# Kernel optimization log

Measured on AMD Instinct MI355X. Metric: run time of the kernel, lower is better.

Reference implementation:

```python
import jax, jax.numpy as jnp
import numpy as np

OMEGA_0 = 30.0  # SIREN frequency from config.kernel.omega_0


def setup_inputs() -> dict:
    key = jax.random.key(0)
    ks = jax.random.split(key, 8)
    B, Ci, Co, L, H = 8, 64, 64, 8192, 32
    x = jax.random.normal(ks[0], (B, Ci, L), dtype=jnp.float32)
    # SIREN-style kernel-net params (Linear(1,H) -> sin -> Linear(H,H) -> sin -> Linear(H, Co*Ci))
    w1 = jax.random.uniform(ks[1], (1, H), jnp.float32, -1.0, 1.0)
    b1 = jax.random.uniform(ks[2], (H,), jnp.float32, -1.0, 1.0)
    c = np.sqrt(6.0 / H) / OMEGA_0
    w2 = jax.random.uniform(ks[3], (H, H), jnp.float32, -c, c)
    b2 = jax.random.uniform(ks[4], (H,), jnp.float32, -c, c)
    w3 = jax.random.uniform(ks[5], (H, Co * Ci), jnp.float32, -c, c)
    b3 = jax.random.uniform(ks[6], (Co * Ci,), jnp.float32, -c, c)
    bias = jnp.zeros((Co,), dtype=jnp.float32)  # CKConv bias init: fill_(0.0)
    return {"x": x, "w1": w1, "b1": b1, "w2": w2, "b2": b2,
            "w3": w3, "b3": b3, "bias": bias}


def reference(x, w1, b1, w2, b2, w3, b3, bias):
    B, Ci, L = x.shape
    Co = bias.shape[0]
    # 1. relative positions in [-1, 1], one per input sample
    rel = jnp.linspace(-1.0, 1.0, L).astype(x.dtype)[:, None]        # (L, 1)
    # 2. SIREN kernel net -> continuous kernel sampled at L positions
    h = jnp.sin(OMEGA_0 * (rel @ w1 + b1))                            # (L, H)
    h = jnp.sin(OMEGA_0 * (h @ w2 + b2))                              # (L, H)
    k = (h @ w3 + b3)                                                 # (L, Co*Ci)
    kernel = k.T.reshape(Co, Ci, L)                                   # (Co, Ci, L)
    # 3. causal full-length conv1d. torch's causal_padding (left zero-pad of
    #    x by K-1, plus a left zero on an even-length kernel) + conv1d
    #    (cross-correlation) is mathematically y[t] = sum_{tau<=t} x[t-tau] *
    #    kernel_flipped[tau], i.e. a causal linear convolution with the
    #    time-reversed kernel. Computed exactly via zero-padded FFT (N=2L >=
    #    L+L-1, so no circular wraparound) instead of O(L^2) direct conv.
    kr = kernel[:, :, ::-1]                                           # flip time axis
    N = 2 * L
    Xf = jnp.fft.rfft(x, n=N, axis=-1)                                # (B, Ci, N/2+1)
    Kf = jnp.fft.rfft(kr, n=N, axis=-1)                               # (Co, Ci, N/2+1)
    Yf = jnp.einsum('bif,oif->bof', Xf, Kf)                           # contract in-channels
    y = jnp.fft.irfft(Yf, n=N, axis=-1)[:, :, :L]                     # (B, Co, L)
    return y + bias[None, :, None]
```

## Files before the change

kernel.cpp:

```cpp
#include <hip/hip_runtime.h>


#define LSEQ   8192
#define N2     8192
#define HDIM   32
#define NB     33
#define NROWS  512
#define NFREQ  8193
#define FSTRIDE 8208
#define FBLK   8
#define FTH    1024
#define OMEGA0 30.0f
#define TWOPI  6.283185307179586f

#define IDX(i) ((i) + ((i) >> 4))
#define BR(k)  ((int)(__brev((unsigned)(k)) >> 19))

__device__ __forceinline__ void build_table(float2* Tq, int tid)
{
    for (int t = tid; t <= 1024; t += FTH) {
        float s, c;
        __sincosf(TWOPI * (float)t / 8192.0f, &s, &c);
        Tq[t] = make_float2(c, s);
    }
}

__device__ __forceinline__ void fft8192_core8(float* re, float* im,
                                              const float2* Tq, int tid)
{
    const float RC = 0.70710678118654752f;
    #pragma unroll
    for (int p = 10; p >= 1; p -= 3) {
        int m = 1 << p;
        int tmul = 1 << (10 - p);
        __syncthreads();
        for (int u = tid; u < 1024; u += FTH) {
            int j = u & (m - 1);
            int base = ((u >> p) << (p + 3)) + j;
            float xr[8], xi[8];
            #pragma unroll
            for (int q = 0; q < 8; ++q) {
                int ix = IDX(base + q * m);
                xr[q] = re[ix]; xi[q] = im[ix];
            }
            float t0r=xr[0]+xr[4], t0i=xi[0]+xi[4];
            float t1r=xr[0]-xr[4], t1i=xi[0]-xi[4];
            float t2r=xr[2]+xr[6], t2i=xi[2]+xi[6];
            float t3r=xr[2]-xr[6], t3i=xi[2]-xi[6];
            float E0r=t0r+t2r, E0i=t0i+t2i;
            float E2r=t0r-t2r, E2i=t0i-t2i;
            float E1r=t1r+t3i, E1i=t1i-t3r;
            float E3r=t1r-t3i, E3i=t1i+t3r;
            float s0r=xr[1]+xr[5], s0i=xi[1]+xi[5];
            float s1r=xr[1]-xr[5], s1i=xi[1]-xi[5];
            float s2r=xr[3]+xr[7], s2i=xi[3]+xi[7];
            float s3r=xr[3]-xr[7], s3i=xi[3]-xi[7];
            float O0r=s0r+s2r, O0i=s0i+s2i;
            float O2r=s0r-s2r, O2i=s0i-s2i;
            float O1r=s1r+s3i, O1i=s1i-s3r;
            float O3r=s1r-s3i, O3i=s1i+s3r;
            float u1r=(O1r+O1i)*RC, u1i=(O1i-O1r)*RC;
            float u2r=O2i,          u2i=-O2r;
            float u3r=(O3i-O3r)*RC, u3i=-(O3r+O3i)*RC;
            float X0r=E0r+O0r, X0i=E0i+O0i;
            float X4r=E0r-O0r, X4i=E0i-O0i;
            float X1r=E1r+u1r, X1i=E1i+u1i;
            float X5r=E1r-u1r, X5i=E1i-u1i;
            float X2r=E2r+u2r, X2i=E2i+u2i;
            float X6r=E2r-u2r, X6i=E2i-u2i;
            float X3r=E3r+u3r, X3i=E3i+u3i;
            float X7r=E3r-u3r, X7i=E3i-u3i;
            float2 tq = Tq[j * tmul];
            float w1r = tq.x,               w1i = -tq.y;
            float w2r = w1r*w1r - w1i*w1i,  w2i = 2.f*w1r*w1i;
            float w3r = w2r*w1r - w2i*w1i,  w3i = w2r*w1i + w2i*w1r;
            float w4r = w2r*w2r - w2i*w2i,  w4i = 2.f*w2r*w2i;
            float w5r = w4r*w1r - w4i*w1i,  w5i = w4r*w1i + w4i*w1r;
            float w6r = w3r*w3r - w3i*w3i,  w6i = 2.f*w3r*w3i;
            float w7r = w4r*w3r - w4i*w3i,  w7i = w4r*w3i + w4i*w3r;
            int i0=IDX(base),       i1=IDX(base+m),   i2=IDX(base+2*m), i3=IDX(base+3*m);
            int i4=IDX(base+4*m),   i5=IDX(base+5*m), i6=IDX(base+6*m), i7=IDX(base+7*m);
            re[i0]=X0r;                     im[i0]=X0i;
            re[i1]=X4r*w4r - X4i*w4i;       im[i1]=X4r*w4i + X4i*w4r;
            re[i2]=X2r*w2r - X2i*w2i;       im[i2]=X2r*w2i + X2i*w2r;
            re[i3]=X6r*w6r - X6i*w6i;       im[i3]=X6r*w6i + X6i*w6r;
            re[i4]=X1r*w1r - X1i*w1i;       im[i4]=X1r*w1i + X1i*w1r;
            re[i5]=X5r*w5r - X5i*w5i;       im[i5]=X5r*w5i + X5i*w5r;
            re[i6]=X3r*w3r - X3i*w3i;       im[i6]=X3r*w3i + X3i*w3r;
            re[i7]=X7r*w7r - X7i*w7i;       im[i7]=X7r*w7i + X7i*w7r;
        }
    }
    __syncthreads();
    for (int u = tid; u < 4096; u += FTH) {
        int a = IDX(2 * u), b = IDX(2 * u + 1);
        float ar = re[a], ai = im[a];
        float br = re[b], bi = im[b];
        re[a] = ar + br; im[a] = ai + bi;
        re[b] = ar - br; im[b] = ai - bi;
    }
    __syncthreads();
}

__global__ __launch_bounds__(FTH) void fwd_kernel(
    const float* __restrict__ x,
    const float* __restrict__ w1, const float* __restrict__ b1,
    const float* __restrict__ w2, const float* __restrict__ b2,
    const float* __restrict__ w3, const float* __restrict__ b3,
    float* __restrict__ Hf, float* __restrict__ XYf, float* __restrict__ M2)
{
    int blk = blockIdx.x;
    int tid = threadIdx.x;

    if (blk >= NB + NROWS) {
        int idx = (blk - (NB + NROWS)) * FTH + tid;
        if (idx < NB * 64 * 64) {
            int o = idx & 63;
            int i = (idx >> 6) & 63;
            int r = idx >> 12;
            M2[idx] = (r < HDIM) ? w3[r * 4096 + o * 64 + i] : b3[o * 64 + i];
        }
        return;
    }

    __shared__ float re[8704], im[8704];
    __shared__ float2 Tq[1025];
    build_table(Tq, tid);

    float* outF;
    long long orow;
    if (blk < NB) {
        int r = blk;
        for (int n = tid; n < 4096; n += FTH) {
            re[IDX(n + 4096)] = 0.0f;  im[IDX(n + 4096)] = 0.0f;
        }
        if (r < HDIM) {
            for (int t = tid; t < LSEQ; t += FTH) {
                float rel = -1.0f + 2.0f * (float)t / (float)(LSEQ - 1);
                float acc = b2[r];
                #pragma unroll 8
                for (int j = 0; j < HDIM; ++j)
                    acc = fmaf(sinf(OMEGA0 * fmaf(rel, w1[j], b1[j])), w2[j * HDIM + r], acc);
                float g = sinf(OMEGA0 * acc);
                int s = LSEQ - 1 - t;
                if (s & 1) im[IDX(s >> 1)] = g;
                else       re[IDX(s >> 1)] = g;
            }
        } else {
            for (int n = tid; n < 4096; n += FTH) {
                re[IDX(n)] = 1.0f;  im[IDX(n)] = 1.0f;
            }
        }
        outF = Hf;  orow = r;
    } else {
        int row = blk - NB;
        const float2* zin = (const float2*)(x + (long long)row * LSEQ);
        for (int n = tid; n < 4096; n += FTH) {
            float2 v = zin[n];
            re[IDX(n)] = v.x;            im[IDX(n)] = v.y;
            re[IDX(n + 4096)] = 0.0f;    im[IDX(n + 4096)] = 0.0f;
        }
        outF = XYf;  orow = row;
    }

    fft8192_core8(re, im, Tq, tid);

    float2* out = (float2*)outF + orow * FSTRIDE;
    for (int k = tid; k <= 8192; k += FTH) {
        int k1 = IDX(BR(k & (N2 - 1)));
        int k2 = IDX(BR((N2 - k) & (N2 - 1)));
        float zr = re[k1], zi = im[k1];
        float wr = re[k2], wi = im[k2];
        float er = 0.5f * (zr + wr), ei = 0.5f * (zi - wi);
        float pr = 0.5f * (zi + wi), pi = 0.5f * (wr - zr);
        float s, c;
        __sincosf(-TWOPI * (float)k / 16384.0f, &s, &c);
        out[k] = make_float2(er + c * pr - s * pi,
                             ei + c * pi + s * pr);
    }
}

__global__ __launch_bounds__(512, 8) void contract_kernel(
    const float* __restrict__ Hf, const float* __restrict__ M2,
    float* __restrict__ XYf)
{
    __shared__ float2 Ks[FBLK][8][64];
    __shared__ __align__(16) float2 Xq[8][8][FBLK];
    int tid = threadIdx.x;
    int o = tid & 63;
    int w = tid >> 6;
    long long f0 = (long long)blockIdx.x * FBLK;

    const float* Hblk = Hf + (size_t)blockIdx.x * (FBLK * 2);

    float2 yacc[FBLK];
    #pragma unroll
    for (int f = 0; f < FBLK; ++f) yacc[f] = make_float2(0.f, 0.f);

    int sf  = tid & 7;
    int sii = (tid >> 3) & 7;
    int sb  = tid >> 6;

    for (int oct = 0; oct < 8; ++oct) {
        __syncthreads();

        const float2* xsrc = (const float2*)XYf
            + (long long)((sb << 6) + (oct << 3) + sii) * FSTRIDE + f0 + sf;
        float2 xstage = *xsrc;

        float2 kacc[FBLK];
        #pragma unroll
        for (int f = 0; f < FBLK; ++f) kacc[f] = make_float2(0.f, 0.f);

        const float* mp = M2 + (((oct << 3) + w) << 6) + o;
        #pragma unroll 3
        for (int r = 0; r < NB; ++r) {
            const float4* hp = (const float4*)(Hblk + (size_t)r * (size_t)(FSTRIDE * 2));
            float4 h0 = hp[0], h1 = hp[1], h2 = hp[2], h3 = hp[3];
            float m0 = mp[r << 12];
            float hr_[FBLK] = {h0.x,h0.z,h1.x,h1.z,h2.x,h2.z,h3.x,h3.z};
            float hi_[FBLK] = {h0.y,h0.w,h1.y,h1.w,h2.y,h2.w,h3.y,h3.w};
            #pragma unroll
            for (int f = 0; f < FBLK; ++f) {
                kacc[f].x = fmaf(m0, hr_[f], kacc[f].x);
                kacc[f].y = fmaf(m0, hi_[f], kacc[f].y);
            }
        }
        Xq[sb][sii][sf] = xstage;
        #pragma unroll
        for (int f = 0; f < FBLK; ++f)
            Ks[f][w][o] = kacc[f];
        __syncthreads();

        #pragma unroll 2
        for (int ii = 0; ii < 8; ++ii) {
            const float4* xp = (const float4*)(&Xq[w][ii][0]);
            float4 x0 = xp[0], x1 = xp[1], x2 = xp[2], x3 = xp[3];
            float xr[FBLK] = {x0.x,x0.z,x1.x,x1.z,x2.x,x2.z,x3.x,x3.z};
            float xi[FBLK] = {x0.y,x0.w,x1.y,x1.w,x2.y,x2.w,x3.y,x3.w};
            #pragma unroll
            for (int f = 0; f < FBLK; ++f) {
                float2 kv = Ks[f][ii][o];
                yacc[f].x = fmaf(xr[f], kv.x, fmaf(-xi[f], kv.y, yacc[f].x));
                yacc[f].y = fmaf(xr[f], kv.y, fmaf( xi[f], kv.x, yacc[f].y));
            }
        }
    }
    __syncthreads();

    long long row = (long long)((w << 6) + o);
    float2* yp = (float2*)XYf + row * FSTRIDE + f0;
    #pragma unroll
    for (int f = 0; f < FBLK; ++f)
        if (f0 + f < NFREQ) yp[f] = yacc[f];
}

__global__ __launch_bounds__(FTH) void irfft_rows_kernel(
    const float* __restrict__ Yf, const float* __restrict__ bias,
    float* __restrict__ out)
{
    __shared__ float re[8704], im[8704];
    __shared__ float2 Tq[1025];
    int tid = threadIdx.x;
    int row = blockIdx.x;
    int o = row & 63;

    build_table(Tq, tid);

    const float2* G = (const float2*)Yf + (long long)row * FSTRIDE;
    for (int k = tid; k < N2; k += FTH) {
        float2 gk = G[k];
        float2 gm = G[8192 - k];
        float er = 0.5f * (gk.x + gm.x), ei = 0.5f * (gk.y - gm.y);
        float pr = 0.5f * (gk.x - gm.x), pi = 0.5f * (gk.y + gm.y);
        float s, c;
        __sincosf(TWOPI * (float)k / 16384.0f, &s, &c);
        float or_ = pr * c - pi * s;
        float oi_ = pr * s + pi * c;
        re[IDX(k)] = er - oi_;
        im[IDX(k)] = -(ei + or_);
    }
    fft8192_core8(re, im, Tq, tid);

    float bo = bias[o];
    const float scale = 1.0f / 8192.0f;
    float2* op = (float2*)(out + (long long)row * LSEQ);
    for (int n = tid; n < 4096; n += FTH) {
        int pn = IDX(BR(n));
        op[n] = make_float2(fmaf(re[pn], scale, bo), fmaf(-im[pn], scale, bo));
    }
}

extern "C" void kernel_launch(void* const* d_in, const int* in_sizes, int n_in,
                              void* d_out, int out_size, void* d_ws, size_t ws_size,
                              hipStream_t stream)
{
    const float* x    = (const float*)d_in[0];
    const float* w1   = (const float*)d_in[1];
    const float* b1   = (const float*)d_in[2];
    const float* w2   = (const float*)d_in[3];
    const float* b2   = (const float*)d_in[4];
    const float* w3   = (const float*)d_in[5];
    const float* b3   = (const float*)d_in[6];
    const float* bias = (const float*)d_in[7];
    float* out = (float*)d_out;

    float* ws  = (float*)d_ws;
    float* Hf  = ws;
    float* M2  = Hf + NB * FSTRIDE * 2;
    float* XYf = M2 + NB * 64 * 64;

    int m2blocks = (NB * 64 * 64 + FTH - 1) / FTH;
    fwd_kernel<<<dim3(NB + NROWS + m2blocks), dim3(FTH), 0, stream>>>(
        x, w1, b1, w2, b2, w3, b3, Hf, XYf, M2);
    contract_kernel<<<dim3((NFREQ + FBLK - 1) / FBLK), dim3(512), 0, stream>>>(Hf, M2, XYf);
    irfft_rows_kernel<<<dim3(NROWS), dim3(FTH), 0, stream>>>(XYf, bias, out);
}
```

Measured before the change: 224.3 us.

## Compute kernel spectra with split-bf16 MFMA instead of scalar FMA loop

The per-frequency kernel-spectrum product (w3/b3 weights times the 33 hidden-unit spectra) now runs on MFMA 16x16x32 bf16 instructions. To keep roughly fp32 accuracy, each operand is split into a high and a low bf16 part and three cross products are summed. The weight matrix is re-laid out as padded 64-row bf16 hi/lo arrays, and the launch bound is relaxed to allow more registers. This trades scalar FMA throughput and repeated global loads for matrix-core work, at the cost of some precision risk and a larger workspace.

```diff
diff --git a/kernel.cpp b/kernel.cpp
--- a/kernel.cpp
+++ b/kernel.cpp
@@ -15,6 +15,19 @@
 
 #define IDX(i) ((i) + ((i) >> 4))
 #define BR(k)  ((int)(__brev((unsigned)(k)) >> 19))
+
+typedef __attribute__((ext_vector_type(8))) short bf16x8;
+typedef __attribute__((ext_vector_type(4))) float f32x4;
+
+__device__ __forceinline__ unsigned short f2bf(float v)
+{
+    unsigned u = __float_as_uint(v);
+    return (unsigned short)((u + 0x7FFFu + ((u >> 16) & 1u)) >> 16);
+}
+__device__ __forceinline__ float bf2f(unsigned short h)
+{
+    return __uint_as_float(((unsigned)h) << 16);
+}
 
 __device__ __forceinline__ void build_table(float2* Tq, int tid)
 {
@@ -106,18 +119,25 @@
     const float* __restrict__ w1, const float* __restrict__ b1,
     const float* __restrict__ w2, const float* __restrict__ b2,
     const float* __restrict__ w3, const float* __restrict__ b3,
-    float* __restrict__ Hf, float* __restrict__ XYf, float* __restrict__ M2)
+    float* __restrict__ Hf, float* __restrict__ XYf,
+    unsigned short* __restrict__ M2hi, unsigned short* __restrict__ M2lo)
 {
     int blk = blockIdx.x;
     int tid = threadIdx.x;
 
     if (blk >= NB + NROWS) {
         int idx = (blk - (NB + NROWS)) * FTH + tid;
-        if (idx < NB * 64 * 64) {
-            int o = idx & 63;
-            int i = (idx >> 6) & 63;
-            int r = idx >> 12;
-            M2[idx] = (r < HDIM) ? w3[r * 4096 + o * 64 + i] : b3[o * 64 + i];
+        if (idx < 4096 * 64) {
+            int r  = idx & 63;
+            int io = idx >> 6;
+            int i  = io >> 6;
+            int o  = io & 63;
+            float v = 0.0f;
+            if (r < HDIM)      v = w3[r * 4096 + o * 64 + i];
+            else if (r == 32)  v = b3[o * 64 + i];
+            unsigned short h = f2bf(v);
+            M2hi[idx] = h;
+            M2lo[idx] = f2bf(v - bf2f(h));
         }
         return;
     }
@@ -179,18 +199,35 @@
     }
 }
 
-__global__ __launch_bounds__(512, 8) void contract_kernel(
-    const float* __restrict__ Hf, const float* __restrict__ M2,
+__global__ __launch_bounds__(512, 4) void contract_kernel(
+    const float* __restrict__ Hf,
+    const unsigned short* __restrict__ M2hi, const unsigned short* __restrict__ M2lo,
     float* __restrict__ XYf)
 {
-    __shared__ float2 Ks[FBLK][8][64];
+    __shared__ float Ks2[FBLK][1036];
     __shared__ __align__(16) float2 Xq[8][8][FBLK];
     int tid = threadIdx.x;
     int o = tid & 63;
     int w = tid >> 6;
+    int lane = tid & 63;
+    int col = lane & 15;
+    int krow0 = (lane >> 4) << 3;
     long long f0 = (long long)blockIdx.x * FBLK;
 
     const float* Hblk = Hf + (size_t)blockIdx.x * (FBLK * 2);
+
+    bf16x8 Bhi[2], Blo[2];
+    #pragma unroll
+    for (int kb = 0; kb < 2; ++kb) {
+        #pragma unroll
+        for (int j = 0; j < 8; ++j) {
+            int r = (kb << 5) + krow0 + j;
+            float v = (r < NB) ? Hblk[(size_t)r * (FSTRIDE * 2) + col] : 0.0f;
+            unsigned short h = f2bf(v);
+            Bhi[kb][j] = (short)h;
+            Blo[kb][j] = (short)f2bf(v - bf2f(h));
+        }
+    }
 
     float2 yacc[FBLK];
     #pragma unroll
@@ -199,6 +236,7 @@
     int sf  = tid & 7;
     int sii = (tid >> 3) & 7;
     int sb  = tid >> 6;
+    int fcol = col >> 1, comp = col & 1;
 
     for (int oct = 0; oct < 8; ++oct) {
         __syncthreads();
@@ -207,28 +245,28 @@
             + (long long)((sb << 6) + (oct << 3) + sii) * FSTRIDE + f0 + sf;
         float2 xstage = *xsrc;
 
-        float2 kacc[FBLK];
+        int iobase = ((oct << 3) + w) << 6;
         #pragma unroll
-        for (int f = 0; f < FBLK; ++f) kacc[f] = make_float2(0.f, 0.f);
-
-        const float* mp = M2 + (((oct << 3) + w) << 6) + o;
-        #pragma unroll 3
-        for (int r = 0; r < NB; ++r) {
-            const float4* hp = (const float4*)(Hblk + (size_t)r * (size_t)(FSTRIDE * 2));
-            float4 h0 = hp[0], h1 = hp[1], h2 = hp[2], h3 = hp[3];
-            float m0 = mp[r << 12];
-            float hr_[FBLK] = {h0.x,h0.z,h1.x,h1.z,h2.x,h2.z,h3.x,h3.z};
-            float hi_[FBLK] = {h0.y,h0.w,h1.y,h1.w,h2.y,h2.w,h3.y,h3.w};
+        for (int tt = 0; tt < 4; ++tt) {
+            size_t abase = ((size_t)(iobase + (tt << 4) + col)) << 6;
+            bf16x8 Ah0 = *(const bf16x8*)(M2hi + abase + krow0);
+            bf16x8 Ah1 = *(const bf16x8*)(M2hi + abase + 32 + krow0);
+            bf16x8 Al0 = *(const bf16x8*)(M2lo + abase + krow0);
+            bf16x8 Al1 = *(const bf16x8*)(M2lo + abase + 32 + krow0);
+            f32x4 acc = {0.f, 0.f, 0.f, 0.f};
+            acc = __builtin_amdgcn_mfma_f32_16x16x32_bf16(Ah0, Bhi[0], acc, 0, 0, 0);
+            acc = __builtin_amdgcn_mfma_f32_16x16x32_bf16(Ah1, Bhi[1], acc, 0, 0, 0);
+            acc = __builtin_amdgcn_mfma_f32_16x16x32_bf16(Ah0, Blo[0], acc, 0, 0, 0);
+            acc = __builtin_amdgcn_mfma_f32_16x16x32_bf16(Ah1, Blo[1], acc, 0, 0, 0);
+            acc = __builtin_amdgcn_mfma_f32_16x16x32_bf16(Al0, Bhi[0], acc, 0, 0, 0);
+            acc = __builtin_amdgcn_mfma_f32_16x16x32_bf16(Al1, Bhi[1], acc, 0, 0, 0);
             #pragma unroll
-            for (int f = 0; f < FBLK; ++f) {
-                kacc[f].x = fmaf(m0, hr_[f], kacc[f].x);
-                kacc[f].y = fmaf(m0, hi_[f], kacc[f].y);
+            for (int p = 0; p < 4; ++p) {
+                int oc = (tt << 4) + ((lane >> 4) << 2) + p;
+                Ks2[fcol][(((w << 6) + oc) << 1) + comp] = acc[p];
             }
         }
         Xq[sb][sii][sf] = xstage;
-        #pragma unroll
-        for (int f = 0; f < FBLK; ++f)
-            Ks[f][w][o] = kacc[f];
         __syncthreads();
 
         #pragma unroll 2
@@ -239,7 +277,7 @@
             float xi[FBLK] = {x0.y,x0.w,x1.y,x1.w,x2.y,x2.w,x3.y,x3.w};
             #pragma unroll
             for (int f = 0; f < FBLK; ++f) {
-                float2 kv = Ks[f][ii][o];
+                float2 kv = *(const float2*)(&Ks2[f][((ii << 6) + o) << 1]);
                 yacc[f].x = fmaf(xr[f], kv.x, fmaf(-xi[f], kv.y, yacc[f].x));
                 yacc[f].y = fmaf(xr[f], kv.y, fmaf( xi[f], kv.x, yacc[f].y));
             }
@@ -306,12 +344,13 @@
 
     float* ws  = (float*)d_ws;
     float* Hf  = ws;
-    float* M2  = Hf + NB * FSTRIDE * 2;
-    float* XYf = M2 + NB * 64 * 64;
-
-    int m2blocks = (NB * 64 * 64 + FTH - 1) / FTH;
+    unsigned short* M2hi = (unsigned short*)(Hf + NB * FSTRIDE * 2);
+    unsigned short* M2lo = M2hi + 4096 * 64;
+    float* XYf = (float*)(M2lo + 4096 * 64);
+
+    int m2blocks = (4096 * 64 + FTH - 1) / FTH;
     fwd_kernel<<<dim3(NB + NROWS + m2blocks), dim3(FTH), 0, stream>>>(
-        x, w1, b1, w2, b2, w3, b3, Hf, XYf, M2);
-    contract_kernel<<<dim3((NFREQ + FBLK - 1) / FBLK), dim3(512), 0, stream>>>(Hf, M2, XYf);
+        x, w1, b1, w2, b2, w3, b3, Hf, XYf, M2hi, M2lo);
+    contract_kernel<<<dim3((NFREQ + FBLK - 1) / FBLK), dim3(512), 0, stream>>>(Hf, M2hi, M2lo, XYf);
     irfft_rows_kernel<<<dim3(NROWS), dim3(FTH), 0, stream>>>(XYf, bias, out);
 }
```

Result: slower. 280.1 us (+24.9%).
